# Kernel tuning notes

Measured on AMD Instinct MI355X. Metric: run time of the kernel, lower is better.

## Reference

```python
import jax, jax.numpy as jnp
import numpy as np

N, IN_C, E = 50000, 512, 800000
H, C = 2, 64          # heads, per-head channels
HC = H * C            # 128
OUT_C = 2
B = 64                # number of graphs
EPS = 1e-5
NEG_SLOPE = 0.2


def gat_conv(x, src, dst, W, a_src, a_dst, bias):
    """PyG GATConv (concat=True, add_self_loops already included in src/dst)."""
    n = x.shape[0]
    h = (x @ W).reshape(n, H, C)                      # [N,H,C]
    alpha_src = (h * a_src[None]).sum(-1)             # [N,H]
    alpha_dst = (h * a_dst[None]).sum(-1)             # [N,H]
    e = jax.nn.leaky_relu(alpha_src[src] + alpha_dst[dst], NEG_SLOPE)  # [E,H]
    # segment softmax over incoming edges of each destination node
    m = jax.ops.segment_max(e, dst, num_segments=n)   # [N,H]
    ex = jnp.exp(e - m[dst])
    denom = jax.ops.segment_sum(ex, dst, num_segments=n)
    alpha = ex / denom[dst]                           # [E,H]
    msg = h[src] * alpha[:, :, None]                  # [E,H,C]
    out = jax.ops.segment_sum(msg, dst, num_segments=n)  # [N,H,C]
    return out.reshape(n, HC) + bias


def batch_norm(x, gamma, beta):
    # BatchNorm1d in training mode: batch statistics over the node dim
    mu = x.mean(0)
    var = x.var(0)
    return gamma * (x - mu) * jax.lax.rsqrt(var + EPS) + beta


def setup_inputs() -> dict:
    key = jax.random.key(0)
    ks = jax.random.split(key, 16)
    x = jax.random.normal(ks[0], (N, IN_C), dtype=jnp.float32)
    edge_index = jax.random.randint(ks[1], (2, E), 0, N, dtype=jnp.int64)
    batch = jnp.sort(jax.random.randint(ks[2], (N,), 0, B, dtype=jnp.int64))
    g = lambda k, sh, fan: jax.random.normal(k, sh, dtype=jnp.float32) * (1.0 / np.sqrt(fan))
    return {
        "x": x, "edge_index": edge_index, "batch": batch,
        "W1": g(ks[3], (IN_C, HC), IN_C),
        "att_src1": g(ks[4], (H, C), C), "att_dst1": g(ks[5], (H, C), C),
        "b1": jnp.zeros((HC,), jnp.float32),
        "gamma1": jnp.ones((HC,), jnp.float32), "beta1": jnp.zeros((HC,), jnp.float32),
        "W2": g(ks[6], (HC, HC), HC),
        "att_src2": g(ks[7], (H, C), C), "att_dst2": g(ks[8], (H, C), C),
        "b2": jnp.zeros((HC,), jnp.float32),
        "gamma2": jnp.ones((HC,), jnp.float32), "beta2": jnp.zeros((HC,), jnp.float32),
        "Wlin": g(ks[9], (HC, OUT_C), HC),
        "blin": jnp.zeros((OUT_C,), jnp.float32),
    }


def reference(x, edge_index, batch, W1, att_src1, att_dst1, b1, gamma1, beta1,
              W2, att_src2, att_dst2, b2, gamma2, beta2, Wlin, blin):
    n = x.shape[0]
    # GATConv adds self-loops by default
    loop = jnp.arange(n, dtype=edge_index.dtype)
    src = jnp.concatenate([edge_index[0], loop])
    dst = jnp.concatenate([edge_index[1], loop])

    h = gat_conv(x, src, dst, W1, att_src1, att_dst1, b1)
    h = jax.nn.relu(batch_norm(h, gamma1, beta1))
    h = gat_conv(h, src, dst, W2, att_src2, att_dst2, b2)
    h = jax.nn.relu(batch_norm(h, gamma2, beta2))

    # global mean pool over graphs
    sums = jax.ops.segment_sum(h, batch, num_segments=B)           # [B,HC]
    cnt = jax.ops.segment_sum(jnp.ones((n,), h.dtype), batch, num_segments=B)
    pooled = sums / jnp.maximum(cnt, 1.0)[:, None]
    return pooled @ Wlin + blin                                    # [B,OUT_C]
```

## Files before the change

kernel.cpp:

```cpp
#include <hip/hip_runtime.h>
#include <hip/hip_bf16.h>
#include <cstdint>
#include <cstddef>

#define NN      50000
#define IN_C    512
#define EE      800000
#define ETOT    850000
#define HH      2
#define CC      64
#define HC      128
#define BB      64
#define OUTC    2
#define NEG_SLOPE 0.2f
#define BN_EPS  1e-5f

#define NBLK_SCAN ((NN + 255) / 256)

#define NXCD     8
#define NPX      ((NN + NXCD - 1) / NXCD)
#define EDGES_PER_SLOT 2048
#define NSLOT    ((ETOT + EDGES_PER_SLOT - 1) / EDGES_PER_SLOT)

typedef __bf16 bf16x8 __attribute__((ext_vector_type(8)));
typedef float  f32x4  __attribute__((ext_vector_type(4)));

__device__ __forceinline__ unsigned f2bf(float f) {
    __bf16 b = (__bf16)f;
    return (unsigned)__builtin_bit_cast(unsigned short, b);
}

__device__ __forceinline__ void gload_lds16(const float* g, float* l) {
    __builtin_amdgcn_global_load_lds(
        (const __attribute__((address_space(1))) unsigned*)g,
        (__attribute__((address_space(3))) unsigned*)l,
        16, 0, 0);
}

__global__ __launch_bounds__(256) void deg_kernel(const int* __restrict__ ei, int* __restrict__ deg)
{
    const int xcd  = blockIdx.x & (NXCD - 1);
    const int slot = blockIdx.x >> 3;
    const int lo = xcd * NPX, hi = lo + NPX;
    const int base = slot * EDGES_PER_SLOT;
#pragma unroll
    for (int it = 0; it < EDGES_PER_SLOT / 256; ++it) {
        int e = base + it * 256 + threadIdx.x;
        if (e < ETOT) {
            int d = (e < EE) ? ei[EE + e] : (e - EE);
            if (d >= lo && d < hi) atomicAdd(&deg[d], 1);
        }
    }
}

__global__ __launch_bounds__(256) void bsum_kernel(const int* __restrict__ deg, int* __restrict__ bsum)
{
    int i = blockIdx.x * 256 + threadIdx.x;
    int v = (i < NN) ? deg[i] : 0;
    int lane = threadIdx.x & 63, wv = threadIdx.x >> 6;
#pragma unroll
    for (int o = 32; o > 0; o >>= 1) v += __shfl_down(v, o);
    __shared__ int ws[4];
    if (lane == 0) ws[wv] = v;
    __syncthreads();
    if (threadIdx.x == 0) bsum[blockIdx.x] = ws[0] + ws[1] + ws[2] + ws[3];
}

__global__ __launch_bounds__(256) void bscan_kernel(
    const int* __restrict__ bsum, int* __restrict__ bofs, int* __restrict__ rowp)
{
    int t = threadIdx.x;
    int lane = t & 63, wv = t >> 6;
    int v = (t < NBLK_SCAN) ? bsum[t] : 0;
    int x = v;
#pragma unroll
    for (int o = 1; o < 64; o <<= 1) {
        int y = __shfl_up(x, o);
        if (lane >= o) x += y;
    }
    __shared__ int ws[4];
    if (lane == 63) ws[wv] = x;
    __syncthreads();
    int wo = 0;
#pragma unroll
    for (int w = 0; w < 4; ++w) if (w < wv) wo += ws[w];
    if (t < NBLK_SCAN) bofs[t] = x + wo - v;
    if (t == 0) rowp[NN] = ETOT;
}

__global__ __launch_bounds__(256) void bapply_kernel(
    const int* __restrict__ deg, const int* __restrict__ bofs,
    int* __restrict__ rowp, int* __restrict__ cur)
{
    int i = blockIdx.x * 256 + threadIdx.x;
    int v = (i < NN) ? deg[i] : 0;
    int lane = threadIdx.x & 63, wv = threadIdx.x >> 6;
    int x = v;
#pragma unroll
    for (int o = 1; o < 64; o <<= 1) {
        int y = __shfl_up(x, o);
        if (lane >= o) x += y;
    }
    __shared__ int ws[4];
    if (lane == 63) ws[wv] = x;
    __syncthreads();
    int wo = 0;
#pragma unroll
    for (int w = 0; w < 4; ++w) if (w < wv) wo += ws[w];
    if (i < NN) {
        int r = bofs[blockIdx.x] + x + wo - v;
        rowp[i] = r; cur[i] = r;
    }
}

__global__ __launch_bounds__(256) void scatter_kernel(
    const int* __restrict__ ei, int* __restrict__ cur, int* __restrict__ esrc)
{
    const int xcd  = blockIdx.x & (NXCD - 1);
    const int slot = blockIdx.x >> 3;
    const int lo = xcd * NPX, hi = lo + NPX;
    const int base = slot * EDGES_PER_SLOT;
#pragma unroll
    for (int it = 0; it < EDGES_PER_SLOT / 256; ++it) {
        int e = base + it * 256 + threadIdx.x;
        if (e < ETOT) {
            int s, d;
            if (e < EE) { s = ei[e]; d = ei[EE + e]; }
            else        { s = e - EE; d = s; }
            if (d >= lo && d < hi) {
                int pos = atomicAdd(&cur[d], 1);
                esrc[pos] = s;
            }
        }
    }
}

__global__ __launch_bounds__(256) void wfrag_kernel(
    const float* __restrict__ W1, unsigned short* __restrict__ Wf1,
    const float* __restrict__ W2, unsigned short* __restrict__ Wf2)
{
    int t = blockIdx.x * 256 + threadIdx.x;
    const float* W; unsigned short* Wf;
    if (t < IN_C * 16) { W = W1; Wf = Wf1; }
    else {
        t -= IN_C * 16;
        if (t >= HC * 16) return;
        W = W2; Wf = Wf2;
    }
    int lane = t & 63, frag = t >> 6;
    int kblk = frag >> 3, nt = frag & 7;
    int quad = lane >> 4, ln = lane & 15;
    int kbase = kblk * 32 + quad * 8;
    int n = nt * 16 + ln;
    unsigned short u[8];
#pragma unroll
    for (int j = 0; j < 8; ++j)
        u[j] = (unsigned short)f2bf(W[(size_t)(kbase + j) * HC + n]);
    ushort4 a; a.x = u[0]; a.y = u[1]; a.z = u[2]; a.w = u[3];
    ushort4 b; b.x = u[4]; b.y = u[5]; b.z = u[6]; b.w = u[7];
    *(ushort4*)(Wf + (size_t)t * 8)     = a;
    *(ushort4*)(Wf + (size_t)t * 8 + 4) = b;
}

template<int K, bool AFFINE>
__global__ __launch_bounds__(256) void mfma_gemm_kernel(
    const float* __restrict__ A, const unsigned short* __restrict__ Wf,
    const float* __restrict__ atts, const float* __restrict__ attd,
    unsigned* __restrict__ hb, float* __restrict__ as_, float* __restrict__ ad_,
    const float* __restrict__ sc, const float* __restrict__ sh)
{
    constexpr int NSTEP = K >> 5;
    __shared__ __align__(16) float Abuf[2][64 * 64];

    const int tid  = threadIdx.x;
    const int wave = tid >> 6, lane = tid & 63;
    const int quad = lane >> 4, ln = lane & 15;
    const int m0 = blockIdx.x * 64;

    const int srow = tid >> 3;
    const int g    = (tid & 7) ^ (srow & 7);
    int grow0 = m0 + srow;      if (grow0 > NN - 1) grow0 = NN - 1;
    int grow1 = m0 + srow + 32; if (grow1 > NN - 1) grow1 = NN - 1;
    const float* gsrc0 = A + (size_t)grow0 * K + g * 4;
    const float* gsrc1 = A + (size_t)grow1 * K + g * 4;

    const int rr = wave * 16 + ln;
    const int base_f = rr * 32;
    const int sA = (((quad * 2)     ^ (rr & 7)) * 4);
    const int sB = (((quad * 2 + 1) ^ (rr & 7)) * 4);

    const unsigned short* wbase = Wf + lane * 8;

    f32x4 acc[8];
#pragma unroll
    for (int nt = 0; nt < 8; ++nt) acc[nt] = (f32x4){0.f, 0.f, 0.f, 0.f};

    gload_lds16(gsrc0,      &Abuf[0][wave * 256]);
    gload_lds16(gsrc1,      &Abuf[0][1024 + wave * 256]);
    gload_lds16(gsrc0 + 32, &Abuf[0][2048 + wave * 256]);
    gload_lds16(gsrc1 + 32, &Abuf[0][3072 + wave * 256]);
    bf16x8 bfr[2][8];
#pragma unroll
    for (int nt = 0; nt < 8; ++nt) bfr[0][nt] = *(const bf16x8*)(wbase + nt * 512);

#pragma unroll
    for (int ks = 0; ks < NSTEP; ++ks) {
        const int sub  = ks & 1;
        const int cbuf = (ks >> 1) & 1;
        const int bsel = ks & 1;
        if (sub == 0) {
            __syncthreads();
            if (ks + 2 < NSTEP) {
                const float* n0 = gsrc0 + (size_t)(ks + 2) * 32;
                const float* n1 = gsrc1 + (size_t)(ks + 2) * 32;
                float* db = &Abuf[cbuf ^ 1][wave * 256];
                gload_lds16(n0,      db);
                gload_lds16(n1,      db + 1024);
                gload_lds16(n0 + 32, db + 2048);
                gload_lds16(n1 + 32, db + 3072);
            }
        }

        const float* fb_base = &Abuf[cbuf][sub * 2048 + base_f];
        float4 fa = *(const float4*)(fb_base + sA);
        float4 fb = *(const float4*)(fb_base + sB);
        float va[8] = {fa.x, fa.y, fa.z, fa.w, fb.x, fb.y, fb.z, fb.w};
        if (AFFINE) {
            const int kk = ks * 32 + quad * 8;
            const float4 s0 = *(const float4*)(sc + kk), s1 = *(const float4*)(sc + kk + 4);
            const float4 h0 = *(const float4*)(sh + kk), h1 = *(const float4*)(sh + kk + 4);
            va[0] = fmaxf(fmaf(s0.x, va[0], h0.x), 0.f);
            va[1] = fmaxf(fmaf(s0.y, va[1], h0.y), 0.f);
            va[2] = fmaxf(fmaf(s0.z, va[2], h0.z), 0.f);
            va[3] = fmaxf(fmaf(s0.w, va[3], h0.w), 0.f);
            va[4] = fmaxf(fmaf(s1.x, va[4], h1.x), 0.f);
            va[5] = fmaxf(fmaf(s1.y, va[5], h1.y), 0.f);
            va[6] = fmaxf(fmaf(s1.z, va[6], h1.z), 0.f);
            va[7] = fmaxf(fmaf(s1.w, va[7], h1.w), 0.f);
        }
        union { bf16x8 v; unsigned short u[8]; } af;
#pragma unroll
        for (int j = 0; j < 8; ++j) af.u[j] = (unsigned short)f2bf(va[j]);

        if (ks + 1 < NSTEP) {
            const unsigned short* wfp = wbase + (size_t)(ks + 1) * 4096;
#pragma unroll
            for (int nt = 0; nt < 8; ++nt)
                bfr[bsel ^ 1][nt] = *(const bf16x8*)(wfp + nt * 512);
        }

#pragma unroll
        for (int nt = 0; nt < 8; ++nt)
            acc[nt] = __builtin_amdgcn_mfma_f32_16x16x32_bf16(af.v, bfr[bsel][nt], acc[nt], 0, 0, 0);
    }

    float wsv[8], wdv[8];
#pragma unroll
    for (int nt = 0; nt < 8; ++nt) { wsv[nt] = atts[nt * 16 + ln]; wdv[nt] = attd[nt * 16 + ln]; }

    const int mbase = m0 + wave * 16 + quad * 4;
#pragma unroll
    for (int r = 0; r < 4; ++r) {
        int m = mbase + r;
        bool ok = (m < NN);
        float ps0 = 0.f, ps1 = 0.f, pd0 = 0.f, pd1 = 0.f;
#pragma unroll
        for (int nt = 0; nt < 8; ++nt) {
            float v = acc[nt][r];
            if (nt < 4) { ps0 = fmaf(v, wsv[nt], ps0); pd0 = fmaf(v, wdv[nt], pd0); }
            else        { ps1 = fmaf(v, wsv[nt], ps1); pd1 = fmaf(v, wdv[nt], pd1); }
        }
#pragma unroll
        for (int nt = 0; nt < 4; ++nt) {
            unsigned pk = f2bf(acc[nt][r]) | (f2bf(acc[nt + 4][r]) << 16);
            if (ok) hb[(size_t)m * 64 + nt * 16 + ln] = pk;
        }
#pragma unroll
        for (int o = 8; o > 0; o >>= 1) {
            ps0 += __shfl_down(ps0, o); ps1 += __shfl_down(ps1, o);
            pd0 += __shfl_down(pd0, o); pd1 += __shfl_down(pd1, o);
        }
        if (ok && ln == 0) {
            *(float2*)&as_[m * 2] = make_float2(ps0, ps1);
            *(float2*)&ad_[m * 2] = make_float2(pd0, pd1);
        }
    }
}

__global__ __launch_bounds__(256) void gat_agg_kernel(
    const int* __restrict__ rowp, const int* __restrict__ esrc,
    const float* __restrict__ as_, const float* __restrict__ ad_,
    const unsigned* __restrict__ hb, float* __restrict__ out,
    float* __restrict__ stats)
{
    const int tid  = threadIdx.x;
    const int node = (blockIdx.x * 256 + tid) >> 6;
    const int wave = tid >> 6;
    const int lane = tid & 63;
    int beg = rowp[node], end = rowp[node + 1];
    float2 adv = *(const float2*)&ad_[node * 2];

    __shared__ __align__(16) float4 stg[4][64];
    float4* sw = stg[wave];

    float l0 = 0.f, l1 = 0.f, a0 = 0.f, a1 = 0.f;

    for (int j0 = beg; j0 < end; j0 += 64) {
        int nj = min(64, end - j0);
        float p0l = 0.f, p1l = 0.f;
        if (j0 + lane < end) {
            int sl = esrc[j0 + lane];
            float2 t = *(const float2*)&as_[sl * 2];
            float e0 = t.x + adv.x; e0 = fmaxf(e0, NEG_SLOPE * e0);
            float e1 = t.y + adv.y; e1 = fmaxf(e1, NEG_SLOPE * e1);
            p0l = __expf(e0); p1l = __expf(e1);
            sw[lane] = make_float4(__int_as_float(sl), p0l, p1l, 0.f);
        }
        l0 += p0l; l1 += p1l;

        int j = 0;
        for (; j + 8 <= nj; j += 8) {
            float4 t0 = sw[j],     t1 = sw[j + 1], t2 = sw[j + 2], t3 = sw[j + 3];
            float4 t4 = sw[j + 4], t5 = sw[j + 5], t6 = sw[j + 6], t7 = sw[j + 7];
            unsigned u0 = hb[(size_t)__float_as_int(t0.x) * 64 + lane];
            unsigned u1 = hb[(size_t)__float_as_int(t1.x) * 64 + lane];
            unsigned u2 = hb[(size_t)__float_as_int(t2.x) * 64 + lane];
            unsigned u3 = hb[(size_t)__float_as_int(t3.x) * 64 + lane];
            unsigned u4 = hb[(size_t)__float_as_int(t4.x) * 64 + lane];
            unsigned u5 = hb[(size_t)__float_as_int(t5.x) * 64 + lane];
            unsigned u6 = hb[(size_t)__float_as_int(t6.x) * 64 + lane];
            unsigned u7 = hb[(size_t)__float_as_int(t7.x) * 64 + lane];
            a0 = fmaf(t0.y, __uint_as_float(u0 << 16), a0);
            a1 = fmaf(t0.z, __uint_as_float(u0 & 0xffff0000u), a1);
            a0 = fmaf(t1.y, __uint_as_float(u1 << 16), a0);
            a1 = fmaf(t1.z, __uint_as_float(u1 & 0xffff0000u), a1);
            a0 = fmaf(t2.y, __uint_as_float(u2 << 16), a0);
            a1 = fmaf(t2.z, __uint_as_float(u2 & 0xffff0000u), a1);
            a0 = fmaf(t3.y, __uint_as_float(u3 << 16), a0);
            a1 = fmaf(t3.z, __uint_as_float(u3 & 0xffff0000u), a1);
            a0 = fmaf(t4.y, __uint_as_float(u4 << 16), a0);
            a1 = fmaf(t4.z, __uint_as_float(u4 & 0xffff0000u), a1);
            a0 = fmaf(t5.y, __uint_as_float(u5 << 16), a0);
            a1 = fmaf(t5.z, __uint_as_float(u5 & 0xffff0000u), a1);
            a0 = fmaf(t6.y, __uint_as_float(u6 << 16), a0);
            a1 = fmaf(t6.z, __uint_as_float(u6 & 0xffff0000u), a1);
            a0 = fmaf(t7.y, __uint_as_float(u7 << 16), a0);
            a1 = fmaf(t7.z, __uint_as_float(u7 & 0xffff0000u), a1);
        }
        for (; j < nj; ++j) {
            float4 t = sw[j];
            unsigned u = hb[(size_t)__float_as_int(t.x) * 64 + lane];
            a0 = fmaf(t.y, __uint_as_float(u << 16), a0);
            a1 = fmaf(t.z, __uint_as_float(u & 0xffff0000u), a1);
        }
    }

#pragma unroll
    for (int o = 1; o < 64; o <<= 1) {
        l0 += __shfl_xor(l0, o); l1 += __shfl_xor(l1, o);
    }
    float v0 = a0 / l0;
    float v1 = a1 / l1;
    out[(size_t)node * HC + lane]      = v0;
    out[(size_t)node * HC + 64 + lane] = v1;

    __shared__ float red[4][256];
    red[wave][lane]      = v0;
    red[wave][64 + lane] = v1;
    __syncthreads();
    if (tid < 128) {
        float s = 0.f, q = 0.f;
#pragma unroll
        for (int w = 0; w < 4; ++w) {
            float v = red[w][tid];
            s += v; q = fmaf(v, v, q);
        }
        int slot = blockIdx.x & 63;
        atomicAdd(&stats[slot * 128 + tid], s);
        atomicAdd(&stats[64 * 128 + slot * 128 + tid], q);
    }
}

__global__ void bn_params_kernel(
    const float* __restrict__ stats, const float* __restrict__ gamma,
    const float* __restrict__ beta, float* __restrict__ sc, float* __restrict__ sh)
{
    int c = threadIdx.x;
    float su = 0.f, sq = 0.f;
#pragma unroll
    for (int k = 0; k < 64; ++k) {
        su += stats[k * 128 + c];
        sq += stats[64 * 128 + k * 128 + c];
    }
    const float inv_n = 1.0f / (float)NN;
    float mu = su * inv_n;
    float var = sq * inv_n - mu * mu;
    float rs = rsqrtf(var + BN_EPS);
    float s = gamma[c] * rs;
    sc[c] = s;
    sh[c] = beta[c] - mu * s;
}

__global__ __launch_bounds__(256) void pool_kernel(
    const float* __restrict__ x, const float* __restrict__ sc,
    const float* __restrict__ sh, const int* __restrict__ batch,
    float* __restrict__ pool, float* __restrict__ cnt)
{
    int c = threadIdx.x & 127;
    int half = threadIdx.x >> 7;
    int r0 = blockIdx.x * 64;
    int rend = min(r0 + 64, NN);
    float s = sc[c], b = sh[c];
    int cur = -1; float acc = 0.f, ccount = 0.f;
    for (int r = r0 + half; r < rend; r += 2) {
        int g = batch[r];
        if (g != cur) {
            if (cur >= 0) {
                atomicAdd(&pool[cur * HC + c], acc);
                if (c == 0) atomicAdd(&cnt[cur], ccount);
            }
            cur = g; acc = 0.f; ccount = 0.f;
        }
        float v = x[(size_t)r * HC + c];
        acc += fmaxf(fmaf(s, v, b), 0.f);
        ccount += 1.f;
    }
    if (cur >= 0) {
        atomicAdd(&pool[cur * HC + c], acc);
        if (c == 0) atomicAdd(&cnt[cur], ccount);
    }
}

__global__ void final_kernel(
    const float* __restrict__ pool, const float* __restrict__ cnt,
    const float* __restrict__ Wlin, const float* __restrict__ blin,
    float* __restrict__ outp)
{
    int t = threadIdx.x;
    int b = t >> 1, oc = t & 1;
    float inv = 1.f / fmaxf(cnt[b], 1.f);
    float s = blin[oc];
    for (int c = 0; c < HC; ++c)
        s += pool[b * HC + c] * inv * Wlin[c * 2 + oc];
    outp[b * 2 + oc] = s;
}

static constexpr size_t OFF_OUT   = 0;
static constexpr size_t OFF_AS    = OFF_OUT + (size_t)NN*HC;
static constexpr size_t OFF_AD    = OFF_AS  + (size_t)NN*HH;
static constexpr size_t OFF_ST1   = OFF_AD  + (size_t)NN*HH;
static constexpr size_t OFF_ST2   = OFF_ST1 + 2*64*128;
static constexpr size_t OFF_SC1   = OFF_ST2 + 2*64*128;
static constexpr size_t OFF_SH1   = OFF_SC1 + 128;
static constexpr size_t OFF_SC2   = OFF_SH1 + 128;
static constexpr size_t OFF_SH2   = OFF_SC2 + 128;
static constexpr size_t OFF_POOL  = OFF_SH2 + 128;
static constexpr size_t OFF_CNT   = OFF_POOL+ (size_t)BB*HC;
static constexpr size_t OFF_ZEND  = OFF_CNT + BB;
static constexpr size_t IOFF_DEG  = 0;
static constexpr size_t IOFF_ROWP = IOFF_DEG  + NN;
static constexpr size_t IOFF_CUR  = IOFF_ROWP + NN + 1;
static constexpr size_t IOFF_BSUM = IOFF_CUR  + NN;
static constexpr size_t IOFF_BOFS = IOFF_BSUM + NBLK_SCAN;
static constexpr size_t IOFF_ESRC = IOFF_BOFS + NBLK_SCAN;
static constexpr size_t IOFF_HB   = (IOFF_ESRC + ETOT + 3) & ~(size_t)3;
static constexpr size_t IOFF_WF1  = IOFF_HB + (size_t)NN*64;
static constexpr size_t IOFF_WF2  = IOFF_WF1 + (size_t)IN_C*64;
static constexpr size_t IOFF_END  = IOFF_WF2 + (size_t)HC*64;

extern "C" void kernel_launch(void* const* d_in, const int* in_sizes, int n_in,
                              void* d_out, int out_size, void* d_ws, size_t ws_size,
                              hipStream_t stream)
{
    const float* x       = (const float*)d_in[0];
    const int*   ei      = (const int*)  d_in[1];
    const int*   batch   = (const int*)  d_in[2];
    const float* W1      = (const float*)d_in[3];
    const float* atts1   = (const float*)d_in[4];
    const float* attd1   = (const float*)d_in[5];
    const float* gamma1  = (const float*)d_in[7];
    const float* beta1   = (const float*)d_in[8];
    const float* W2      = (const float*)d_in[9];
    const float* atts2   = (const float*)d_in[10];
    const float* attd2   = (const float*)d_in[11];
    const float* gamma2  = (const float*)d_in[13];
    const float* beta2   = (const float*)d_in[14];
    const float* Wlin    = (const float*)d_in[15];
    const float* blin    = (const float*)d_in[16];
    float* outp = (float*)d_out;

    float* ws    = (float*)d_ws;
    float* out   = ws + OFF_OUT;
    float* as_   = ws + OFF_AS;
    float* ad_   = ws + OFF_AD;
    float* st1   = ws + OFF_ST1;
    float* st2   = ws + OFF_ST2;
    float* sc1   = ws + OFF_SC1;
    float* sh1   = ws + OFF_SH1;
    float* sc2   = ws + OFF_SC2;
    float* sh2   = ws + OFF_SH2;
    float* pool  = ws + OFF_POOL;
    float* cnt   = ws + OFF_CNT;

    int* iws  = (int*)(ws + OFF_ZEND);
    int* deg  = iws + IOFF_DEG;
    int* rowp = iws + IOFF_ROWP;
    int* curp = iws + IOFF_CUR;
    int* bsum = iws + IOFF_BSUM;
    int* bofs = iws + IOFF_BOFS;
    int* esrc = iws + IOFF_ESRC;
    unsigned* hb = (unsigned*)(iws + IOFF_HB);
    unsigned short* Wf1 = (unsigned short*)(iws + IOFF_WF1);
    unsigned short* Wf2 = (unsigned short*)(iws + IOFF_WF2);

    const int BIN_BLK   = NXCD * NSLOT;
    const int GEMM_BLK  = (NN + 63) / 64;
    const int WAVE_BLK  = (NN + 3) / 4;
    const int POOL_BLK  = (NN + 63) / 64;
    const int WFRG_BLK  = (IN_C * 16 + HC * 16 + 255) / 256;

    hipMemsetAsync(st1, 0, (OFF_ZEND - OFF_ST1) * sizeof(float) + NN * sizeof(int), stream);

    wfrag_kernel<<<WFRG_BLK, 256, 0, stream>>>(W1, Wf1, W2, Wf2);
    deg_kernel<<<BIN_BLK, 256, 0, stream>>>(ei, deg);
    bsum_kernel<<<NBLK_SCAN, 256, 0, stream>>>(deg, bsum);
    bscan_kernel<<<1, 256, 0, stream>>>(bsum, bofs, rowp);
    bapply_kernel<<<NBLK_SCAN, 256, 0, stream>>>(deg, bofs, rowp, curp);
    scatter_kernel<<<BIN_BLK, 256, 0, stream>>>(ei, curp, esrc);

    mfma_gemm_kernel<IN_C, false><<<GEMM_BLK, 256, 0, stream>>>(
        x, Wf1, atts1, attd1, hb, as_, ad_, nullptr, nullptr);
    gat_agg_kernel<<<WAVE_BLK, 256, 0, stream>>>(rowp, esrc, as_, ad_, hb, out, st1);
    bn_params_kernel<<<1, 128, 0, stream>>>(st1, gamma1, beta1, sc1, sh1);

    mfma_gemm_kernel<HC, true><<<GEMM_BLK, 256, 0, stream>>>(
        out, Wf2, atts2, attd2, hb, as_, ad_, sc1, sh1);
    gat_agg_kernel<<<WAVE_BLK, 256, 0, stream>>>(rowp, esrc, as_, ad_, hb, out, st2);
    bn_params_kernel<<<1, 128, 0, stream>>>(st2, gamma2, beta2, sc2, sh2);

    pool_kernel<<<POOL_BLK, 256, 0, stream>>>(out, sc2, sh2, batch, pool, cnt);
    final_kernel<<<1, 128, 0, stream>>>(pool, cnt, Wlin, blin, outp);
}
```

Before: 435.9 us.

## Process two nodes per wave in GAT aggregation with 8-byte gathers

The aggregation kernel now assigns each half-wave (32 lanes) to one destination node, so a 64-lane wave handles two nodes. Each lane gathers a uint2 (four bf16 channels) per source row instead of one 32-bit word. Edge indices and weights are broadcast with shuffles rather than staged through shared memory. The aim is to halve per-node wave overhead, use wider memory transactions and drop LDS traffic. The cost is idle lanes when the two nodes in a wave have different degrees, plus the block count now assumes NN is divisible by 8.

Result: faster. 417.5 us (-4.2%).

```diff
diff --git a/kernel.cpp b/kernel.cpp
--- a/kernel.cpp
+++ b/kernel.cpp
@@ -294,84 +294,87 @@
     float* __restrict__ stats)
 {
     const int tid  = threadIdx.x;
-    const int node = (blockIdx.x * 256 + tid) >> 6;
     const int wave = tid >> 6;
     const int lane = tid & 63;
-    int beg = rowp[node], end = rowp[node + 1];
+    const int half = lane >> 5;
+    const int hl   = lane & 31;
+    const int node = blockIdx.x * 8 + wave * 2 + half;
+
+    const int beg = rowp[node], end = rowp[node + 1];
     float2 adv = *(const float2*)&ad_[node * 2];
 
-    __shared__ __align__(16) float4 stg[4][64];
-    float4* sw = stg[wave];
-
-    float l0 = 0.f, l1 = 0.f, a0 = 0.f, a1 = 0.f;
-
-    for (int j0 = beg; j0 < end; j0 += 64) {
-        int nj = min(64, end - j0);
-        float p0l = 0.f, p1l = 0.f;
-        if (j0 + lane < end) {
-            int sl = esrc[j0 + lane];
+    const int deg = end - beg;
+    const int degmax = max(deg, __shfl_xor(deg, 32));
+    const int nchunk = (degmax + 31) >> 5;
+    const int sb = half * 32;
+    const unsigned* hbp = hb + 2 * hl;
+
+    float l0 = 0.f, l1 = 0.f;
+    float a00 = 0.f, a01 = 0.f, a10 = 0.f, a11 = 0.f;
+
+    for (int c = 0; c < nchunk; ++c) {
+        int j0 = beg + c * 32;
+        int sl = 0; float p0l = 0.f, p1l = 0.f;
+        if (j0 + hl < end) {
+            sl = esrc[j0 + hl];
             float2 t = *(const float2*)&as_[sl * 2];
             float e0 = t.x + adv.x; e0 = fmaxf(e0, NEG_SLOPE * e0);
             float e1 = t.y + adv.y; e1 = fmaxf(e1, NEG_SLOPE * e1);
             p0l = __expf(e0); p1l = __expf(e1);
-            sw[lane] = make_float4(__int_as_float(sl), p0l, p1l, 0.f);
         }
         l0 += p0l; l1 += p1l;
 
+        int nj = end - j0; nj = nj < 0 ? 0 : (nj > 32 ? 32 : nj);
+        int njmax = max(nj, __shfl_xor(nj, 32));
+
         int j = 0;
-        for (; j + 8 <= nj; j += 8) {
-            float4 t0 = sw[j],     t1 = sw[j + 1], t2 = sw[j + 2], t3 = sw[j + 3];
-            float4 t4 = sw[j + 4], t5 = sw[j + 5], t6 = sw[j + 6], t7 = sw[j + 7];
-            unsigned u0 = hb[(size_t)__float_as_int(t0.x) * 64 + lane];
-            unsigned u1 = hb[(size_t)__float_as_int(t1.x) * 64 + lane];
-            unsigned u2 = hb[(size_t)__float_as_int(t2.x) * 64 + lane];
-            unsigned u3 = hb[(size_t)__float_as_int(t3.x) * 64 + lane];
-            unsigned u4 = hb[(size_t)__float_as_int(t4.x) * 64 + lane];
-            unsigned u5 = hb[(size_t)__float_as_int(t5.x) * 64 + lane];
-            unsigned u6 = hb[(size_t)__float_as_int(t6.x) * 64 + lane];
-            unsigned u7 = hb[(size_t)__float_as_int(t7.x) * 64 + lane];
-            a0 = fmaf(t0.y, __uint_as_float(u0 << 16), a0);
-            a1 = fmaf(t0.z, __uint_as_float(u0 & 0xffff0000u), a1);
-            a0 = fmaf(t1.y, __uint_as_float(u1 << 16), a0);
-            a1 = fmaf(t1.z, __uint_as_float(u1 & 0xffff0000u), a1);
-            a0 = fmaf(t2.y, __uint_as_float(u2 << 16), a0);
-            a1 = fmaf(t2.z, __uint_as_float(u2 & 0xffff0000u), a1);
-            a0 = fmaf(t3.y, __uint_as_float(u3 << 16), a0);
-            a1 = fmaf(t3.z, __uint_as_float(u3 & 0xffff0000u), a1);
-            a0 = fmaf(t4.y, __uint_as_float(u4 << 16), a0);
-            a1 = fmaf(t4.z, __uint_as_float(u4 & 0xffff0000u), a1);
-            a0 = fmaf(t5.y, __uint_as_float(u5 << 16), a0);
-            a1 = fmaf(t5.z, __uint_as_float(u5 & 0xffff0000u), a1);
-            a0 = fmaf(t6.y, __uint_as_float(u6 << 16), a0);
-            a1 = fmaf(t6.z, __uint_as_float(u6 & 0xffff0000u), a1);
-            a0 = fmaf(t7.y, __uint_as_float(u7 << 16), a0);
-            a1 = fmaf(t7.z, __uint_as_float(u7 & 0xffff0000u), a1);
-        }
-        for (; j < nj; ++j) {
-            float4 t = sw[j];
-            unsigned u = hb[(size_t)__float_as_int(t.x) * 64 + lane];
-            a0 = fmaf(t.y, __uint_as_float(u << 16), a0);
-            a1 = fmaf(t.z, __uint_as_float(u & 0xffff0000u), a1);
-        }
-    }
-
-#pragma unroll
-    for (int o = 1; o < 64; o <<= 1) {
+        for (; j + 8 <= njmax; j += 8) {
+            uint2 u[8]; float p0[8], p1[8];
+#pragma unroll
+            for (int q = 0; q < 8; ++q) {
+                int s  = __shfl(sl, sb + j + q);
+                p0[q]  = __shfl(p0l, sb + j + q);
+                p1[q]  = __shfl(p1l, sb + j + q);
+                u[q]   = *(const uint2*)(hbp + (size_t)s * 64);
+            }
+#pragma unroll
+            for (int q = 0; q < 8; ++q) {
+                a00 = fmaf(p0[q], __uint_as_float(u[q].x << 16), a00);
+                a10 = fmaf(p1[q], __uint_as_float(u[q].x & 0xffff0000u), a10);
+                a01 = fmaf(p0[q], __uint_as_float(u[q].y << 16), a01);
+                a11 = fmaf(p1[q], __uint_as_float(u[q].y & 0xffff0000u), a11);
+            }
+        }
+        for (; j < njmax; ++j) {
+            int s  = __shfl(sl, sb + j);
+            float p0 = __shfl(p0l, sb + j);
+            float p1 = __shfl(p1l, sb + j);
+            uint2 u = *(const uint2*)(hbp + (size_t)s * 64);
+            a00 = fmaf(p0, __uint_as_float(u.x << 16), a00);
+            a10 = fmaf(p1, __uint_as_float(u.x & 0xffff0000u), a10);
+            a01 = fmaf(p0, __uint_as_float(u.y << 16), a01);
+            a11 = fmaf(p1, __uint_as_float(u.y & 0xffff0000u), a11);
+        }
+    }
+
+#pragma unroll
+    for (int o = 1; o < 32; o <<= 1) {
         l0 += __shfl_xor(l0, o); l1 += __shfl_xor(l1, o);
     }
-    float v0 = a0 / l0;
-    float v1 = a1 / l1;
-    out[(size_t)node * HC + lane]      = v0;
-    out[(size_t)node * HC + 64 + lane] = v1;
-
-    __shared__ float red[4][256];
-    red[wave][lane]      = v0;
-    red[wave][64 + lane] = v1;
+    float r0 = 1.f / l0, r1 = 1.f / l1;
+    float v00 = a00 * r0, v01 = a01 * r0, v10 = a10 * r1, v11 = a11 * r1;
+    *(float2*)&out[(size_t)node * HC + 2 * hl]      = make_float2(v00, v01);
+    *(float2*)&out[(size_t)node * HC + 64 + 2 * hl] = make_float2(v10, v11);
+
+    __shared__ float red[8][128];
+    const int w2 = wave * 2 + half;
+    red[w2][2 * hl]      = v00;  red[w2][2 * hl + 1]      = v01;
+    red[w2][64 + 2 * hl] = v10;  red[w2][64 + 2 * hl + 1] = v11;
     __syncthreads();
     if (tid < 128) {
         float s = 0.f, q = 0.f;
 #pragma unroll
-        for (int w = 0; w < 4; ++w) {
+        for (int w = 0; w < 8; ++w) {
             float v = red[w][tid];
             s += v; q = fmaf(v, v, q);
         }
@@ -515,7 +518,7 @@
 
     const int BIN_BLK   = NXCD * NSLOT;
     const int GEMM_BLK  = (NN + 63) / 64;
-    const int WAVE_BLK  = (NN + 3) / 4;
+    const int WAVE_BLK  = NN / 8;
     const int POOL_BLK  = (NN + 63) / 64;
     const int WFRG_BLK  = (IN_C * 16 + HC * 16 + 255) / 256;
 
```
